# Kernel optimization log

Measured on AMD Instinct MI355X. Metric: run time of the kernel, lower is better.

## Reference

```python
import jax, jax.numpy as jnp
import numpy as np

B, S, H, D = 2, 2048, 16, 64

def setup_inputs() -> dict:
    key = jax.random.key(0)
    kq, kk, kv = jax.random.split(key, 3)
    q = jax.random.normal(kq, (B, S, H, D), dtype=jnp.float32)
    k = jax.random.normal(kk, (B, S, H, D), dtype=jnp.float32)
    v = jax.random.normal(kv, (B, S, H, D), dtype=jnp.float32)
    return {"q": q, "k": k, "v": v}

def reference(q, k, v):
    # q, k, v: [B, S, H, D]; single-process path == full softmax attention,
    # which is exactly what the ring online-softmax computes over all chunks.
    d = q.shape[-1]
    scale = 1.0 / jnp.sqrt(jnp.asarray(d, dtype=q.dtype))
    # scores: [B, H, Sq, Sk]
    scores = jnp.einsum("bqhd,bkhd->bhqk", q, k) * scale
    attn = jax.nn.softmax(scores, axis=-1)
    # output back in [B, S, H, D] layout (torch transposes back)
    out = jnp.einsum("bhqk,bkhd->bqhd", attn, v)
    return out
```

## Files before the change

### kernel.cpp

```cpp
#include <hip/hip_runtime.h>
#include <hip/hip_bf16.h>

namespace {

constexpr int Sseq = 2048;
constexpr int NH   = 16;
constexpr int HD   = 64;
constexpr int ROW  = NH * HD;
constexpr int BM   = 128;
constexpr int BN   = 64;
constexpr int MT   = 2;
constexpr int NT   = Sseq / BN;
constexpr float QSCALE = 0.18033688011112042f;

typedef __bf16 bf16_t;
typedef __attribute__((ext_vector_type(8))) bf16_t bf16x8;
typedef __attribute__((ext_vector_type(4))) float f32x4;
typedef __attribute__((ext_vector_type(2))) unsigned int u32x2;
typedef __attribute__((ext_vector_type(4))) unsigned int u32x4;

union Frag { bf16x8 v; unsigned int u[4]; };

__device__ inline unsigned int pkbf(float a, float b) {
  union { __hip_bfloat162 h; unsigned int u; } x;
  x.h = __float22bfloat162_rn(make_float2(a, b));
  return x.u;
}


__global__ __launch_bounds__(256)
void fa_fwd(const float* __restrict__ Q, const float* __restrict__ K,
            const float* __restrict__ V, float* __restrict__ O) {
  const int id   = blockIdx.x;
  const int bh   = id & 31;
  const int qblk = id >> 5;
  const int tid  = threadIdx.x;
  const int wave = tid >> 6;
  const int lane = tid & 63;
  const int qd   = lane >> 4;
  const int lm   = lane & 15;

  const size_t base = (size_t)(bh >> 4) * Sseq * ROW + (size_t)(bh & 15) * HD;
  const float* qb = Q + base;
  const float* kb = K + base;
  const float* vb = V + base;
  float*       ob = O + base;

  __shared__ __align__(16) unsigned short KT[2][HD * 64];
  __shared__ __align__(16) unsigned short VT[2][HD * 64];
  __shared__ __align__(16) unsigned short PB[4][MT][16 * 64];

  const int qrow0 = qblk * BM + wave * (MT * 16);

  Frag qf[MT][2];
  for (int mt = 0; mt < MT; ++mt) {
    const float* qp = qb + (size_t)(qrow0 + mt * 16 + lm) * ROW;
    for (int ks = 0; ks < 2; ++ks) {
      f32x4 a = *(const f32x4*)(qp + ks * 32 + qd * 8);
      f32x4 c = *(const f32x4*)(qp + ks * 32 + qd * 8 + 4);
      qf[mt][ks].u[0] = pkbf(a[0] * QSCALE, a[1] * QSCALE);
      qf[mt][ks].u[1] = pkbf(a[2] * QSCALE, a[3] * QSCALE);
      qf[mt][ks].u[2] = pkbf(c[0] * QSCALE, c[1] * QSCALE);
      qf[mt][ks].u[3] = pkbf(c[2] * QSCALE, c[3] * QSCALE);
    }
  }

  f32x4 oacc[MT][4] = {};
  float lsum[MT] = {};

  const int kr = tid >> 2;
  const int kd = (tid & 3) * 16;
  const int n4 = (tid & 15) * 4;
  const int d4 = (tid >> 4) * 4;

  const float* kpA = kb + (size_t)kr * ROW + kd;
  const float* vpA = vb + (size_t)n4 * ROW + d4;
  const float* kpB = kpA + (size_t)BN * ROW;
  const float* vpB = vpA + (size_t)BN * ROW;

  f32x4 ka[4], va[4], kB[4], vB[4];

  auto ldK = [&](const float* p, f32x4* r) {
    r[0] = *(const f32x4*)(p);
    r[1] = *(const f32x4*)(p + 4);
    r[2] = *(const f32x4*)(p + 8);
    r[3] = *(const f32x4*)(p + 12);
  };
  auto ldV = [&](const float* p, f32x4* r) {
    r[0] = *(const f32x4*)(p);
    r[1] = *(const f32x4*)(p + ROW);
    r[2] = *(const f32x4*)(p + 2 * ROW);
    r[3] = *(const f32x4*)(p + 3 * ROW);
  };

  auto stage = [&](unsigned short* kt, unsigned short* vt,
                   const f32x4* kx, const f32x4* vx) {
    {
      int c0 = ((tid & 3) * 2) ^ (kr & 7);
      int c1 = ((tid & 3) * 2 + 1) ^ (kr & 7);
      u32x4 w0, w1;
      w0.x = pkbf(kx[0][0], kx[0][1]); w0.y = pkbf(kx[0][2], kx[0][3]);
      w0.z = pkbf(kx[1][0], kx[1][1]); w0.w = pkbf(kx[1][2], kx[1][3]);
      w1.x = pkbf(kx[2][0], kx[2][1]); w1.y = pkbf(kx[2][2], kx[2][3]);
      w1.z = pkbf(kx[3][0], kx[3][1]); w1.w = pkbf(kx[3][2], kx[3][3]);
      *(u32x4*)(kt + kr * 64 + c0 * 8) = w0;
      *(u32x4*)(kt + kr * 64 + c1 * 8) = w1;
    }
    {
      #pragma unroll
      for (int i = 0; i < 4; ++i) {
        int d = d4 + i;
        int chunk = (n4 >> 3) ^ (d & 7);
        u32x2 val; val.x = pkbf(vx[0][i], vx[1][i]); val.y = pkbf(vx[2][i], vx[3][i]);
        *(u32x2*)(vt + d * 64 + chunk * 8 + (n4 & 7)) = val;
      }
    }
  };

  auto compute = [&](const unsigned short* kt, const unsigned short* vt) {
    #pragma unroll
    for (int c = 0; c < 4; ++c) {
      Frag kf0, kf1;
      {
        int r = c * 16 + lm;
        int ch0 = (qd) ^ (lm & 7);
        int ch1 = (4 + qd) ^ (lm & 7);
        kf0.v = *(const bf16x8*)(kt + r * 64 + ch0 * 8);
        kf1.v = *(const bf16x8*)(kt + r * 64 + ch1 * 8);
      }
      #pragma unroll
      for (int mt = 0; mt < MT; ++mt) {
        f32x4 s = {};
        s = __builtin_amdgcn_mfma_f32_16x16x32_bf16(kf0.v, qf[mt][0].v, s, 0, 0, 0);
        s = __builtin_amdgcn_mfma_f32_16x16x32_bf16(kf1.v, qf[mt][1].v, s, 0, 0, 0);
        float e0 = __builtin_amdgcn_exp2f(s[0]);
        float e1 = __builtin_amdgcn_exp2f(s[1]);
        float e2 = __builtin_amdgcn_exp2f(s[2]);
        float e3 = __builtin_amdgcn_exp2f(s[3]);
        lsum[mt] += (e0 + e1) + (e2 + e3);
        int n = c * 16 + qd * 4;
        int chunk = (n >> 3) ^ (lm & 7);
        u32x2 val; val.x = pkbf(e0, e1); val.y = pkbf(e2, e3);
        *(u32x2*)(PB[wave][mt] + lm * 64 + chunk * 8 + (n & 7)) = val;
      }
    }

    __threadfence_block();

    #pragma unroll
    for (int ks = 0; ks < 2; ++ks) {
      bf16x8 pfr[MT];
      #pragma unroll
      for (int mt = 0; mt < MT; ++mt) {
        int chunk = (ks * 4 + qd) ^ (lm & 7);
        pfr[mt] = *(const bf16x8*)(PB[wave][mt] + lm * 64 + chunk * 8);
      }
      #pragma unroll
      for (int dt = 0; dt < 4; ++dt) {
        int d = dt * 16 + lm;
        int chunk = (ks * 4 + qd) ^ (d & 7);
        bf16x8 vf = *(const bf16x8*)(vt + d * 64 + chunk * 8);
        #pragma unroll
        for (int mt = 0; mt < MT; ++mt)
          oacc[mt][dt] = __builtin_amdgcn_mfma_f32_16x16x32_bf16(vf, pfr[mt], oacc[mt][dt], 0, 0, 0);
      }
    }
  };

  ldK(kpA, ka); ldV(vpA, va);
  ldK(kpB, kB); ldV(vpB, vB);

  for (int t = 0; t < NT; t += 2) {
    stage(KT[0], VT[0], ka, va);
    __syncthreads();
    if (t + 2 < NT) {
      kpA += (size_t)2 * BN * ROW; vpA += (size_t)2 * BN * ROW;
      ldK(kpA, ka); ldV(vpA, va);
    }
    compute(KT[0], VT[0]);

    stage(KT[1], VT[1], kB, vB);
    __syncthreads();
    if (t + 3 < NT) {
      kpB += (size_t)2 * BN * ROW; vpB += (size_t)2 * BN * ROW;
      ldK(kpB, kB); ldV(vpB, vB);
    }
    compute(KT[1], VT[1]);
  }

  #pragma unroll
  for (int mt = 0; mt < MT; ++mt) {
    float l = lsum[mt];
    l += __shfl_xor(l, 16, 64);
    l += __shfl_xor(l, 32, 64);
    float r = 1.0f / l;
    float* op = ob + (size_t)(qrow0 + mt * 16 + lm) * ROW + qd * 4;
    #pragma unroll
    for (int dt = 0; dt < 4; ++dt) {
      f32x4 o = oacc[mt][dt];
      o[0] *= r; o[1] *= r; o[2] *= r; o[3] *= r;
      *(f32x4*)(op + dt * 16) = o;
    }
  }
}

}

extern "C" void kernel_launch(void* const* d_in, const int* in_sizes, int n_in,
                              void* d_out, int out_size, void* d_ws, size_t ws_size,
                              hipStream_t stream) {
  const float* q = (const float*)d_in[0];
  const float* k = (const float*)d_in[1];
  const float* v = (const float*)d_in[2];
  float* o = (float*)d_out;
  (void)in_sizes; (void)n_in; (void)out_size; (void)d_ws; (void)ws_size;
  dim3 grid(2 * NH * (Sseq / BM));
  dim3 block(256);
  hipLaunchKernelGGL(fa_fwd, grid, block, 0, stream, q, k, v, o);
}
```

Before: 140.8 us.

## Split key tiles across wave pairs in 512-thread blocks and reduce partial outputs in LDS

Blocks grow from 4 to 8 waves. Each pair of waves shares a 32-row query group and splits every 64-key tile in half: each wave computes scores, exponentials and the PV product for its own 32 keys. The K and V global loads are also split, with one half of the threads loading K and the other half loading V. At the end, the partial outputs and row sums of one wave in each pair go through shared memory (reusing the K/V tile buffers) and are combined before normalising and storing. The aim is more resident waves per CU to hide memory and MFMA latency, at the cost of an extra synchronised reduction and higher register pressure under the new launch bounds.

```diff
diff --git a/kernel.cpp b/kernel.cpp
--- a/kernel.cpp
+++ b/kernel.cpp
@@ -28,7 +28,7 @@
 }
 
 
-__global__ __launch_bounds__(256)
+__global__ __launch_bounds__(512, 4)
 void fa_fwd(const float* __restrict__ Q, const float* __restrict__ K,
             const float* __restrict__ V, float* __restrict__ O) {
   const int id   = blockIdx.x;
@@ -39,6 +39,8 @@
   const int lane = tid & 63;
   const int qd   = lane >> 4;
   const int lm   = lane & 15;
+  const int qg   = wave >> 1;
+  const int kg   = wave & 1;
 
   const size_t base = (size_t)(bh >> 4) * Sseq * ROW + (size_t)(bh & 15) * HD;
   const float* qb = Q + base;
@@ -50,7 +52,7 @@
   __shared__ __align__(16) unsigned short VT[2][HD * 64];
   __shared__ __align__(16) unsigned short PB[4][MT][16 * 64];
 
-  const int qrow0 = qblk * BM + wave * (MT * 16);
+  const int qrow0 = qblk * BM + qg * (MT * 16);
 
   Frag qf[MT][2];
   for (int mt = 0; mt < MT; ++mt) {
@@ -68,50 +70,50 @@
   f32x4 oacc[MT][4] = {};
   float lsum[MT] = {};
 
-  const int kr = tid >> 2;
-  const int kd = (tid & 3) * 16;
-  const int n4 = (tid & 15) * 4;
-  const int d4 = (tid >> 4) * 4;
-
-  const float* kpA = kb + (size_t)kr * ROW + kd;
-  const float* vpA = vb + (size_t)n4 * ROW + d4;
-  const float* kpB = kpA + (size_t)BN * ROW;
-  const float* vpB = vpA + (size_t)BN * ROW;
-
-  f32x4 ka[4], va[4], kB[4], vB[4];
-
-  auto ldK = [&](const float* p, f32x4* r) {
-    r[0] = *(const f32x4*)(p);
-    r[1] = *(const f32x4*)(p + 4);
-    r[2] = *(const f32x4*)(p + 8);
-    r[3] = *(const f32x4*)(p + 12);
+  const bool isK = tid < 256;
+  const int stid = tid & 255;
+  const int kr = stid >> 2;
+  const int kd = (stid & 3) * 16;
+  const int n4 = (stid & 15) * 4;
+  const int d4 = (stid >> 4) * 4;
+
+  const float* gpA = isK ? kb + (size_t)kr * ROW + kd
+                         : vb + (size_t)n4 * ROW + d4;
+  const float* gpB = gpA + (size_t)BN * ROW;
+
+  f32x4 ra[4], rb[4];
+
+  auto ld = [&](const float* p, f32x4* r) {
+    if (isK) {
+      r[0] = *(const f32x4*)(p);
+      r[1] = *(const f32x4*)(p + 4);
+      r[2] = *(const f32x4*)(p + 8);
+      r[3] = *(const f32x4*)(p + 12);
+    } else {
+      r[0] = *(const f32x4*)(p);
+      r[1] = *(const f32x4*)(p + ROW);
+      r[2] = *(const f32x4*)(p + 2 * ROW);
+      r[3] = *(const f32x4*)(p + 3 * ROW);
+    }
   };
-  auto ldV = [&](const float* p, f32x4* r) {
-    r[0] = *(const f32x4*)(p);
-    r[1] = *(const f32x4*)(p + ROW);
-    r[2] = *(const f32x4*)(p + 2 * ROW);
-    r[3] = *(const f32x4*)(p + 3 * ROW);
-  };
-
-  auto stage = [&](unsigned short* kt, unsigned short* vt,
-                   const f32x4* kx, const f32x4* vx) {
-    {
-      int c0 = ((tid & 3) * 2) ^ (kr & 7);
-      int c1 = ((tid & 3) * 2 + 1) ^ (kr & 7);
+
+  auto stage = [&](unsigned short* kt, unsigned short* vt, const f32x4* x) {
+    if (isK) {
+      int c0 = ((stid & 3) * 2) ^ (kr & 7);
+      int c1 = ((stid & 3) * 2 + 1) ^ (kr & 7);
       u32x4 w0, w1;
-      w0.x = pkbf(kx[0][0], kx[0][1]); w0.y = pkbf(kx[0][2], kx[0][3]);
-      w0.z = pkbf(kx[1][0], kx[1][1]); w0.w = pkbf(kx[1][2], kx[1][3]);
-      w1.x = pkbf(kx[2][0], kx[2][1]); w1.y = pkbf(kx[2][2], kx[2][3]);
-      w1.z = pkbf(kx[3][0], kx[3][1]); w1.w = pkbf(kx[3][2], kx[3][3]);
+      w0.x = pkbf(x[0][0], x[0][1]); w0.y = pkbf(x[0][2], x[0][3]);
+      w0.z = pkbf(x[1][0], x[1][1]); w0.w = pkbf(x[1][2], x[1][3]);
+      w1.x = pkbf(x[2][0], x[2][1]); w1.y = pkbf(x[2][2], x[2][3]);
+      w1.z = pkbf(x[3][0], x[3][1]); w1.w = pkbf(x[3][2], x[3][3]);
       *(u32x4*)(kt + kr * 64 + c0 * 8) = w0;
       *(u32x4*)(kt + kr * 64 + c1 * 8) = w1;
-    }
-    {
+    } else {
       #pragma unroll
       for (int i = 0; i < 4; ++i) {
         int d = d4 + i;
         int chunk = (n4 >> 3) ^ (d & 7);
-        u32x2 val; val.x = pkbf(vx[0][i], vx[1][i]); val.y = pkbf(vx[2][i], vx[3][i]);
+        u32x2 val; val.x = pkbf(x[0][i], x[1][i]); val.y = pkbf(x[2][i], x[3][i]);
         *(u32x2*)(vt + d * 64 + chunk * 8 + (n4 & 7)) = val;
       }
     }
@@ -119,7 +121,8 @@
 
   auto compute = [&](const unsigned short* kt, const unsigned short* vt) {
     #pragma unroll
-    for (int c = 0; c < 4; ++c) {
+    for (int cc = 0; cc < 2; ++cc) {
+      const int c = kg * 2 + cc;
       Frag kf0, kf1;
       {
         int r = c * 16 + lm;
@@ -141,19 +144,19 @@
         int n = c * 16 + qd * 4;
         int chunk = (n >> 3) ^ (lm & 7);
         u32x2 val; val.x = pkbf(e0, e1); val.y = pkbf(e2, e3);
-        *(u32x2*)(PB[wave][mt] + lm * 64 + chunk * 8 + (n & 7)) = val;
+        *(u32x2*)(PB[qg][mt] + lm * 64 + chunk * 8 + (n & 7)) = val;
       }
     }
 
     __threadfence_block();
 
-    #pragma unroll
-    for (int ks = 0; ks < 2; ++ks) {
+    {
+      const int ks = kg;
       bf16x8 pfr[MT];
       #pragma unroll
       for (int mt = 0; mt < MT; ++mt) {
         int chunk = (ks * 4 + qd) ^ (lm & 7);
-        pfr[mt] = *(const bf16x8*)(PB[wave][mt] + lm * 64 + chunk * 8);
+        pfr[mt] = *(const bf16x8*)(PB[qg][mt] + lm * 64 + chunk * 8);
       }
       #pragma unroll
       for (int dt = 0; dt < 4; ++dt) {
@@ -167,39 +170,61 @@
     }
   };
 
-  ldK(kpA, ka); ldV(vpA, va);
-  ldK(kpB, kB); ldV(vpB, vB);
+  ld(gpA, ra); ld(gpB, rb);
 
   for (int t = 0; t < NT; t += 2) {
-    stage(KT[0], VT[0], ka, va);
+    stage(KT[0], VT[0], ra);
     __syncthreads();
     if (t + 2 < NT) {
-      kpA += (size_t)2 * BN * ROW; vpA += (size_t)2 * BN * ROW;
-      ldK(kpA, ka); ldV(vpA, va);
+      gpA += (size_t)2 * BN * ROW;
+      ld(gpA, ra);
     }
     compute(KT[0], VT[0]);
 
-    stage(KT[1], VT[1], kB, vB);
+    stage(KT[1], VT[1], rb);
     __syncthreads();
     if (t + 3 < NT) {
-      kpB += (size_t)2 * BN * ROW; vpB += (size_t)2 * BN * ROW;
-      ldK(kpB, kB); ldV(vpB, vB);
+      gpB += (size_t)2 * BN * ROW;
+      ld(gpB, rb);
     }
     compute(KT[1], VT[1]);
   }
 
-  #pragma unroll
-  for (int mt = 0; mt < MT; ++mt) {
-    float l = lsum[mt];
-    l += __shfl_xor(l, 16, 64);
-    l += __shfl_xor(l, 32, 64);
-    float r = 1.0f / l;
-    float* op = ob + (size_t)(qrow0 + mt * 16 + lm) * ROW + qd * 4;
+  __syncthreads();
+  float* redO = reinterpret_cast<float*>(qg < 2 ? &KT[0][0] : &VT[0][0])
+              + (size_t)(qg & 1) * 2048;
+  if (kg == 1) {
     #pragma unroll
-    for (int dt = 0; dt < 4; ++dt) {
-      f32x4 o = oacc[mt][dt];
-      o[0] *= r; o[1] *= r; o[2] *= r; o[3] *= r;
-      *(f32x4*)(op + dt * 16) = o;
+    for (int mt = 0; mt < MT; ++mt) {
+      float l = lsum[mt];
+      l += __shfl_xor(l, 16, 64);
+      l += __shfl_xor(l, 32, 64);
+      if (lane < 16) reinterpret_cast<float*>(&PB[qg][mt][0])[lane] = l;
+      #pragma unroll
+      for (int dt = 0; dt < 4; ++dt)
+        *(f32x4*)(redO + ((mt * 4 + dt) * 64 + lane) * 4) = oacc[mt][dt];
+    }
+  }
+  __syncthreads();
+  if (kg == 0) {
+    #pragma unroll
+    for (int mt = 0; mt < MT; ++mt) {
+      float l = lsum[mt];
+      l += __shfl_xor(l, 16, 64);
+      l += __shfl_xor(l, 32, 64);
+      l += reinterpret_cast<float*>(&PB[qg][mt][0])[lm];
+      float r = 1.0f / l;
+      float* op = ob + (size_t)(qrow0 + mt * 16 + lm) * ROW + qd * 4;
+      #pragma unroll
+      for (int dt = 0; dt < 4; ++dt) {
+        f32x4 o = oacc[mt][dt];
+        f32x4 o2 = *(const f32x4*)(redO + ((mt * 4 + dt) * 64 + lane) * 4);
+        o[0] = (o[0] + o2[0]) * r;
+        o[1] = (o[1] + o2[1]) * r;
+        o[2] = (o[2] + o2[2]) * r;
+        o[3] = (o[3] + o2[3]) * r;
+        *(f32x4*)(op + dt * 16) = o;
+      }
     }
   }
 }
@@ -215,6 +240,6 @@
   float* o = (float*)d_out;
   (void)in_sizes; (void)n_in; (void)out_size; (void)d_ws; (void)ws_size;
   dim3 grid(2 * NH * (Sseq / BM));
-  dim3 block(256);
+  dim3 block(512);
   hipLaunchKernelGGL(fa_fwd, grid, block, 0, stream, q, k, v, o);
 }
```

New measurement: 175.4 us. +24.6%, slower.

## Split KV sequence across two blocks with combine kernel

Applied to the files above, without the earlier changes.

Splits the key/value sequence into two halves so each query tile is processed by two blocks (1024 blocks instead of 512), writing unnormalized partial outputs and row sums to workspace. A second kernel adds the partials and normalizes. The aim is to fill more of the GPU's compute units. The cost is extra global traffic for the partials, a second launch, and reliance on workspace being provided. The no-max softmax trick makes the combine a plain sum.

```diff
diff --git a/kernel.cpp b/kernel.cpp
--- a/kernel.cpp
+++ b/kernel.cpp
@@ -30,10 +30,15 @@
 
 __global__ __launch_bounds__(256)
 void fa_fwd(const float* __restrict__ Q, const float* __restrict__ K,
-            const float* __restrict__ V, float* __restrict__ O) {
+            const float* __restrict__ V, float* __restrict__ O,
+            float* __restrict__ Opart, float* __restrict__ Lpart) {
   const int id   = blockIdx.x;
-  const int bh   = id & 31;
-  const int qblk = id >> 5;
+  const int half = id >> 9;
+  const int rem  = id & 511;
+  const bool split = (gridDim.x > 512);
+  const int ntl  = split ? (NT / 2) : NT;
+  const int bh   = rem & 31;
+  const int qblk = rem >> 5;
   const int tid  = threadIdx.x;
   const int wave = tid >> 6;
   const int lane = tid & 63;
@@ -41,9 +46,10 @@
   const int lm   = lane & 15;
 
   const size_t base = (size_t)(bh >> 4) * Sseq * ROW + (size_t)(bh & 15) * HD;
+  const size_t kvoff = (size_t)(half * (NT / 2)) * BN * ROW;
   const float* qb = Q + base;
-  const float* kb = K + base;
-  const float* vb = V + base;
+  const float* kb = K + base + kvoff;
+  const float* vb = V + base + kvoff;
   float*       ob = O + base;
 
   __shared__ __align__(16) unsigned short KT[2][HD * 64];
@@ -170,10 +176,10 @@
   ldK(kpA, ka); ldV(vpA, va);
   ldK(kpB, kB); ldV(vpB, vB);
 
-  for (int t = 0; t < NT; t += 2) {
+  for (int t = 0; t < ntl; t += 2) {
     stage(KT[0], VT[0], ka, va);
     __syncthreads();
-    if (t + 2 < NT) {
+    if (t + 2 < ntl) {
       kpA += (size_t)2 * BN * ROW; vpA += (size_t)2 * BN * ROW;
       ldK(kpA, ka); ldV(vpA, va);
     }
@@ -181,27 +187,64 @@
 
     stage(KT[1], VT[1], kB, vB);
     __syncthreads();
-    if (t + 3 < NT) {
+    if (t + 3 < ntl) {
       kpB += (size_t)2 * BN * ROW; vpB += (size_t)2 * BN * ROW;
       ldK(kpB, kB); ldV(vpB, vB);
     }
     compute(KT[1], VT[1]);
   }
 
-  #pragma unroll
-  for (int mt = 0; mt < MT; ++mt) {
-    float l = lsum[mt];
-    l += __shfl_xor(l, 16, 64);
-    l += __shfl_xor(l, 32, 64);
-    float r = 1.0f / l;
-    float* op = ob + (size_t)(qrow0 + mt * 16 + lm) * ROW + qd * 4;
-    #pragma unroll
-    for (int dt = 0; dt < 4; ++dt) {
-      f32x4 o = oacc[mt][dt];
-      o[0] *= r; o[1] *= r; o[2] *= r; o[3] *= r;
-      *(f32x4*)(op + dt * 16) = o;
-    }
-  }
+  if (!split) {
+    #pragma unroll
+    for (int mt = 0; mt < MT; ++mt) {
+      float l = lsum[mt];
+      l += __shfl_xor(l, 16, 64);
+      l += __shfl_xor(l, 32, 64);
+      float r = 1.0f / l;
+      float* op = ob + (size_t)(qrow0 + mt * 16 + lm) * ROW + qd * 4;
+      #pragma unroll
+      for (int dt = 0; dt < 4; ++dt) {
+        f32x4 o = oacc[mt][dt];
+        o[0] *= r; o[1] *= r; o[2] *= r; o[3] *= r;
+        *(f32x4*)(op + dt * 16) = o;
+      }
+    }
+  } else {
+    const size_t TOT = (size_t)2 * Sseq * NH * HD;
+    const int    NR  = 2 * Sseq * NH;
+    #pragma unroll
+    for (int mt = 0; mt < MT; ++mt) {
+      float l = lsum[mt];
+      l += __shfl_xor(l, 16, 64);
+      l += __shfl_xor(l, 32, 64);
+      if (lane < 16)
+        Lpart[(size_t)half * NR +
+              ((size_t)(bh >> 4) * Sseq + qrow0 + mt * 16 + lane) * NH + (bh & 15)] = l;
+      float* op = Opart + (size_t)half * TOT + base +
+                  (size_t)(qrow0 + mt * 16 + lm) * ROW + qd * 4;
+      #pragma unroll
+      for (int dt = 0; dt < 4; ++dt)
+        *(f32x4*)(op + dt * 16) = oacc[mt][dt];
+    }
+  }
+}
+
+__global__ __launch_bounds__(256)
+void fa_combine(const float* __restrict__ Opart, const float* __restrict__ Lpart,
+                float* __restrict__ O) {
+  const size_t TOT = (size_t)2 * Sseq * NH * HD;
+  const int    NR  = 2 * Sseq * NH;
+  const int t = blockIdx.x * 256 + threadIdx.x;
+  const int row = t >> 4;
+  const float r = 1.0f / (Lpart[row] + Lpart[row + NR]);
+  const f32x4 a = *(const f32x4*)(Opart + (size_t)t * 4);
+  const f32x4 b = *(const f32x4*)(Opart + TOT + (size_t)t * 4);
+  f32x4 o;
+  o[0] = (a[0] + b[0]) * r;
+  o[1] = (a[1] + b[1]) * r;
+  o[2] = (a[2] + b[2]) * r;
+  o[3] = (a[3] + b[3]) * r;
+  *(f32x4*)(O + (size_t)t * 4) = o;
 }
 
 }
@@ -213,8 +256,22 @@
   const float* k = (const float*)d_in[1];
   const float* v = (const float*)d_in[2];
   float* o = (float*)d_out;
-  (void)in_sizes; (void)n_in; (void)out_size; (void)d_ws; (void)ws_size;
-  dim3 grid(2 * NH * (Sseq / BM));
-  dim3 block(256);
-  hipLaunchKernelGGL(fa_fwd, grid, block, 0, stream, q, k, v, o);
-}
+  (void)in_sizes; (void)n_in; (void)out_size;
+
+  const size_t TOT  = (size_t)2 * Sseq * NH * HD;
+  const size_t NRT  = (size_t)2 * 2 * Sseq * NH;
+  const size_t need = (2 * TOT + NRT) * sizeof(float);
+
+  float* Opart = (float*)d_ws;
+  float* Lpart = Opart ? Opart + 2 * TOT : nullptr;
+
+  if (d_ws != nullptr && ws_size >= need) {
+    hipLaunchKernelGGL(fa_fwd, dim3(1024), dim3(256), 0, stream,
+                       q, k, v, o, Opart, Lpart);
+    hipLaunchKernelGGL(fa_combine, dim3((unsigned)(TOT / 4 / 256)), dim3(256),
+                       0, stream, Opart, Lpart, o);
+  } else {
+    hipLaunchKernelGGL(fa_fwd, dim3(512), dim3(256), 0, stream,
+                       q, k, v, o, Opart, Lpart);
+  }
+}
```

After: 158.5 us. +12.6%, slower.
